# Optimization experiments

Hardware: AMD Instinct MI355X
Metric: run time of the kernel (lower is better)

Reference implementation:

```python
import jax, jax.numpy as jnp
import numpy as np

B, S, D = 4, 2048, 1024


def setup_inputs() -> dict:
    key = jax.random.key(0)
    ks = jax.random.split(key, 9)
    scale = 1.0 / np.sqrt(D)
    x = jax.random.normal(ks[0], (B, S, D), dtype=jnp.float32)
    # causal mask (batch, seq, seq), int32; positions with 0 are masked out
    mask = jnp.broadcast_to(jnp.tril(jnp.ones((S, S), dtype=jnp.int32)), (B, S, S))
    Wq = jax.random.uniform(ks[1], (D, D), jnp.float32, -scale, scale)
    bq = jax.random.uniform(ks[2], (D,), jnp.float32, -scale, scale)
    Wk = jax.random.uniform(ks[3], (D, D), jnp.float32, -scale, scale)
    bk = jax.random.uniform(ks[4], (D,), jnp.float32, -scale, scale)
    Wv = jax.random.uniform(ks[5], (D, D), jnp.float32, -scale, scale)
    bv = jax.random.uniform(ks[6], (D,), jnp.float32, -scale, scale)
    Wo = jax.random.uniform(ks[7], (D, D), jnp.float32, -scale, scale)
    bo = jax.random.uniform(ks[8], (D,), jnp.float32, -scale, scale)
    return {"x": x, "mask": mask, "Wq": Wq, "bq": bq, "Wk": Wk, "bk": bk,
            "Wv": Wv, "bv": bv, "Wo": Wo, "bo": bo}


def reference(x, mask, Wq, bq, Wk, bk, Wv, bv, Wo, bo):
    d_model = x.shape[-1]
    scaling = jnp.sqrt(jnp.asarray(d_model, dtype=jnp.float32))
    # torch nn.Linear: y = x @ W.T + b
    Q = jnp.einsum('bsd,ed->bse', x, Wq) + bq
    K = jnp.einsum('bsd,ed->bse', x, Wk) + bk
    V = jnp.einsum('bsd,ed->bse', x, Wv) + bv
    scores = jnp.einsum('bqd,bkd->bqk', Q, K) / scaling  # (B, S, S)
    scores = jnp.where(mask == 0, jnp.float32(-1e9), scores)
    attn = jax.nn.softmax(scores, axis=2)
    out = jnp.einsum('bqk,bkd->bqd', attn, V)
    out = jnp.einsum('bsd,ed->bse', out, Wo) + bo
    return out, attn
```

## Files before the change

kernel.cpp:

```cpp
#include <hip/hip_runtime.h>
#include <hip/hip_bf16.h>
#include <stdint.h>


typedef unsigned short u16;
typedef __attribute__((ext_vector_type(8))) __bf16 bf16x8;
typedef __attribute__((ext_vector_type(4))) float f32x4;

__device__ __forceinline__ u16 f2bf(float f) {
  unsigned int u = __builtin_bit_cast(unsigned int, f);
  u = u + 0x7FFFu + ((u >> 16) & 1u);
  return (u16)(u >> 16);
}

__device__ __forceinline__ float bf2f(u16 u) {
  unsigned int w = ((unsigned int)u) << 16;
  return __builtin_bit_cast(float, w);
}

__device__ __forceinline__ void gl_lds16(const void* g, void* l) {
  __builtin_amdgcn_global_load_lds(
      (const __attribute__((address_space(1))) void*)g,
      (__attribute__((address_space(3))) void*)l, 16, 0, 0);
}

#define MFMA(a, b, c) __builtin_amdgcn_mfma_f32_16x16x32_bf16((a), (b), (c), 0, 0, 0)

#define TILE 128
#define BKK  64
template<int GM, int GX, int OUTMODE, bool BIAS, bool CKB, int NTT>
__global__ __launch_bounds__(256) void gemm_bt(
    const u16* __restrict__ A, const u16* __restrict__ Bmat,
    const float* __restrict__ b0, const float* __restrict__ b1,
    const float* __restrict__ b2,
    void* __restrict__ C0, u16* __restrict__ C1, u16* __restrict__ C2,
    int N, int K, long long sAb, long long sBb, long long sCb, int nchunk,
    const u16* __restrict__ A6, const u16* __restrict__ B6,
    u16* __restrict__ C6) {
  __shared__ __align__(16) u16 As[2][TILE * BKK];
  __shared__ __align__(16) u16 Bs[2][TILE * BKK];
  const int bid = blockIdx.x;
  int bx, by, bz;
  int role6 = 0;
  if (GM == 1) {
    const int lidx = (bid & 7) * nchunk + (bid >> 3);
    bz = lidx / 136;
    const int i = lidx - bz * 136;
    by = (int)((sqrtf(8.f * i + 1.f) - 1.f) * 0.5f);
    while ((by + 1) * (by + 2) / 2 <= i) ++by;
    while (by * (by + 1) / 2 > i) --by;
    bx = i - by * (by + 1) / 2;
  } else if (GM == 3) {
    const int j = bid & 255;
    const int k = j >> 5;
    by = (bid >> 8) ? k : 15 - k;
    bz = (j & 31) >> 3;
    bx = j & 7;
  } else if (GM == 4) {
    const int xcd = bid & 7, c = bid >> 3;
    bz = 0;
    by = xcd * 8 + (c >> 3);
    bx = c & 7;
  } else {
    const int lidx = (bid & 7) * nchunk + (bid >> 3);
    if (lidx < 544) {
      bz = lidx / 136;
      const int i = lidx - bz * 136;
      by = (int)((sqrtf(8.f * i + 1.f) - 1.f) * 0.5f);
      while ((by + 1) * (by + 2) / 2 <= i) ++by;
      while (by * (by + 1) / 2 > i) --by;
      bx = i - by * (by + 1) / 2;
    } else {
      role6 = 1;
      const int v = lidx - 544;
      bz = v >> 7;
      by = (v & 127) >> 4;
      bx = v & 15;
    }
  }
  const int t = threadIdx.x;
  const int lane = t & 63, wid = t >> 6;
  const int wm = (wid >> 1) * 64, wn = (wid & 1) * 64;
  const int fr = lane & 15, fh = lane >> 4;

  const u16* Aeff = A;
  const u16* Beff = Bmat;
  u16* C0e = (u16*)C0;
  long long sAe = sAb, sBe = sBb, sCe = sCb;
  if (GM == 6 && role6) {
    Aeff = A6; Beff = B6; C0e = C6;
    sAe = 0;
    sCe = (long long)1024 * 2048;
  }

  const char* Ab = (const char*)(Aeff + (size_t)bz * sAe + (size_t)by * TILE * K);
  const size_t rowstride = (size_t)K * 2;
  const size_t BOFF = (size_t)8 * TILE * rowstride;
  const char* Btile = (const char*)(Beff + (size_t)bz * sBe + (size_t)bx * TILE * K);

  int srow[4], scol[4], slin[4];
#pragma unroll
  for (int c = 0; c < 4; ++c) {
    slin[c] = c * 4096 + t * 16;
    srow[c] = slin[c] >> 7;
    scol[c] = (slin[c] & 127) ^ ((srow[c] & 7) << 4);
  }

  int Keff = K;
  if (CKB) { int kb2 = (by + 1) * TILE; Keff = kb2 < K ? kb2 : K; }
  const int nkt = Keff / BKK;

#define STAGE(ko_, buf_, Bp_)                                                 \
  {                                                                           \
    _Pragma("unroll") for (int c = 0; c < 4; ++c) {                           \
      gl_lds16(Ab + (size_t)srow[c] * rowstride + (ko_) + scol[c],            \
               (char*)As[buf_] + slin[c]);                                    \
      gl_lds16((Bp_) + (size_t)srow[c] * rowstride + (ko_) + scol[c],         \
               (char*)Bs[buf_] + slin[c]);                                    \
    }                                                                         \
  }

  STAGE(0, 0, Btile)
  __syncthreads();

  int cur = 0;
  for (int tt = 0; tt < NTT; ++tt) {
    f32x4 acc[4][4];
#pragma unroll
    for (int m = 0; m < 4; ++m)
#pragma unroll
      for (int n = 0; n < 4; ++n) acc[m][n] = {0.f, 0.f, 0.f, 0.f};

    for (int kt = 0; kt < nkt; ++kt) {
      const bool last = (kt + 1 == nkt);
      if (!last) {
        STAGE((size_t)(kt + 1) * (BKK * 2), cur ^ 1, Btile)
      } else if (NTT > 1 && tt + 1 < NTT) {
        STAGE(0, cur ^ 1, Btile + BOFF)
      }
      const char* Ac = (const char*)As[cur];
      const char* Bc = (const char*)Bs[cur];
#pragma unroll
      for (int kk = 0; kk < BKK; kk += 32) {
        bf16x8 af[4], bg[4];
#pragma unroll
        for (int m = 0; m < 4; ++m) {
          int r = wm + m * 16 + fr;
          int cb = (kk * 2 + fh * 16) ^ ((r & 7) << 4);
          af[m] = *(const bf16x8*)(Ac + r * 128 + cb);
        }
#pragma unroll
        for (int n = 0; n < 4; ++n) {
          int r = wn + n * 16 + fr;
          int cb = (kk * 2 + fh * 16) ^ ((r & 7) << 4);
          bg[n] = *(const bf16x8*)(Bc + r * 128 + cb);
        }
#pragma unroll
        for (int m = 0; m < 4; ++m)
#pragma unroll
          for (int n = 0; n < 4; ++n)
            acc[m][n] = MFMA(af[m], bg[n], acc[m][n]);
      }
      if (!last) __syncthreads();
      cur ^= 1;
    }

    const int bxe = bx + 8 * tt;
    const int gm0 = by * TILE + wm, gn0 = bxe * TILE + wn;
#pragma unroll
    for (int n = 0; n < 4; ++n) {
      const int gc = gn0 + n * 16 + fr;
      float bvv = 0.f;
      if (BIAS) {
        if (OUTMODE == 3) {
          const int w = bxe >> 3;
          bvv = (w == 0 ? b0 : w == 1 ? b1 : b2)[gc & 1023];
        } else {
          bvv = b0[gc];
        }
      }
#pragma unroll
      for (int m = 0; m < 4; ++m) {
        const int gr0 = gm0 + m * 16 + fh * 4;
        float v[4];
#pragma unroll
        for (int j = 0; j < 4; ++j) v[j] = acc[m][n][j] + bvv;
        if (OUTMODE == 1) {
          float* C = (float*)C0 + (size_t)bz * sCb;
#pragma unroll
          for (int j = 0; j < 4; ++j) C[(size_t)(gr0 + j) * N + gc] = v[j];
        } else if (OUTMODE == 0) {
          u16* C = C0e + (size_t)bz * sCe;
#pragma unroll
          for (int j = 0; j < 4; ++j) C[(size_t)(gr0 + j) * N + gc] = f2bf(v[j]);
        } else {
          const int w = bxe >> 3;
          const int gcl = gc & 1023;
          u16* dst = (w == 0) ? (u16*)C0 : (w == 1) ? C1 : C2;
          const float sc = (w == 0) ? 0.03125f : 1.0f;
#pragma unroll
          for (int j = 0; j < 4; ++j)
            dst[(size_t)(gr0 + j) * 1024 + gcl] = f2bf(v[j] * sc);
        }
      }
    }

    if (NTT > 1 && tt + 1 < NTT) {
      __syncthreads();
      Btile += BOFF;
    }
  }
#undef STAGE
}

__global__ __launch_bounds__(256) void cvt_all(
    const float4* __restrict__ x, ushort4* __restrict__ xb,
    const float4* __restrict__ w0, const float4* __restrict__ w1,
    const float4* __restrict__ w2, const float4* __restrict__ w3,
    ushort4* __restrict__ o0, ushort4* __restrict__ o1,
    ushort4* __restrict__ o2, ushort4* __restrict__ o3) {
  int i = blockIdx.x * 256 + threadIdx.x;
  const float4* src;
  ushort4* dst;
  int idx;
  if (i < 2097152) {
    src = x; dst = xb; idx = i;
  } else {
    int j = i - 2097152;
    int w = j >> 18;
    idx = j & 262143;
    src = (w == 0) ? w0 : (w == 1) ? w1 : (w == 2) ? w2 : w3;
    dst = (w == 0) ? o0 : (w == 1) ? o1 : (w == 2) ? o2 : o3;
  }
  float4 v = src[idx];
  ushort4 o;
  o.x = f2bf(v.x); o.y = f2bf(v.y); o.z = f2bf(v.z); o.w = f2bf(v.w);
  dst[idx] = o;
}

__global__ __launch_bounds__(256) void softmax_rows(
    u16* __restrict__ pb, float* __restrict__ attnF) {
  const int row = blockIdx.x;
  const int q = row & 2047;
  const int nv = q + 1;
  const int nvt = (q & ~127) + 128;
  const int t = threadIdx.x;
  u16* brow = pb + (size_t)row * 2048;
  float* srow = attnF + (size_t)row * 2048;
  __shared__ float red[4];

  const int e0 = 8 * t;
  float a[8];
  if (e0 < nvt) {
    ushort4 u0 = ((const ushort4*)brow)[2 * t];
    ushort4 u1 = ((const ushort4*)brow)[2 * t + 1];
    u16 us[8] = {u0.x, u0.y, u0.z, u0.w, u1.x, u1.y, u1.z, u1.w};
#pragma unroll
    for (int j = 0; j < 8; ++j)
      a[j] = (e0 + j < nv) ? bf2f(us[j]) : -3.0e38f;
  } else {
#pragma unroll
    for (int j = 0; j < 8; ++j) a[j] = -3.0e38f;
  }

  float lmax = -3.0e38f;
#pragma unroll
  for (int j = 0; j < 8; ++j) lmax = fmaxf(lmax, a[j]);
#pragma unroll
  for (int o = 32; o > 0; o >>= 1) lmax = fmaxf(lmax, __shfl_xor(lmax, o));
  if ((t & 63) == 0) red[t >> 6] = lmax;
  __syncthreads();
  const float m = fmaxf(fmaxf(red[0], red[1]), fmaxf(red[2], red[3]));
  __syncthreads();

  float lsum = 0.f;
#pragma unroll
  for (int j = 0; j < 8; ++j) {
    a[j] = __expf(a[j] - m);
    lsum += a[j];
  }
#pragma unroll
  for (int o = 32; o > 0; o >>= 1) lsum += __shfl_xor(lsum, o);
  if ((t & 63) == 0) red[t >> 6] = lsum;
  __syncthreads();
  const float inv = 1.f / (red[0] + red[1] + red[2] + red[3]);

#pragma unroll
  for (int j = 0; j < 8; ++j) a[j] *= inv;
  ((float4*)srow)[2 * t]     = float4{a[0], a[1], a[2], a[3]};
  ((float4*)srow)[2 * t + 1] = float4{a[4], a[5], a[6], a[7]};
  if (e0 < nvt) {
    ushort4 ba; ba.x = f2bf(a[0]); ba.y = f2bf(a[1]); ba.z = f2bf(a[2]); ba.w = f2bf(a[3]);
    ushort4 bb; bb.x = f2bf(a[4]); bb.y = f2bf(a[5]); bb.z = f2bf(a[6]); bb.w = f2bf(a[7]);
    ((ushort4*)brow)[2 * t]     = ba;
    ((ushort4*)brow)[2 * t + 1] = bb;
  }
}

extern "C" void kernel_launch(void* const* d_in, const int* in_sizes, int n_in,
                              void* d_out, int out_size, void* d_ws,
                              size_t ws_size, hipStream_t stream) {
  (void)in_sizes; (void)n_in; (void)out_size; (void)ws_size;
  const int B = 4, S = 2048, D = 1024;
  const float* x  = (const float*)d_in[0];
  const float* Wq = (const float*)d_in[2]; const float* bq = (const float*)d_in[3];
  const float* Wk = (const float*)d_in[4]; const float* bk = (const float*)d_in[5];
  const float* Wv = (const float*)d_in[6]; const float* bv = (const float*)d_in[7];
  const float* Wo = (const float*)d_in[8]; const float* bo = (const float*)d_in[9];

  float* out  = (float*)d_out;
  float* attn = out + (size_t)B * S * D;

  char* ws = (char*)d_ws;
  u16* xb  = (u16*)(ws);
  u16* wqb = (u16*)(ws + 16777216);
  u16* wkb = wqb + 1048576;
  u16* wvb = wkb + 1048576;
  u16* wob = wvb + 1048576;
  u16* qb  = (u16*)(ws + 25165824);
  u16* kb  = (u16*)(ws + 41943040);
  u16* vr  = (u16*)(ws + 58720256);
  u16* pb  = (u16*)(ws + 75497472);

  cvt_all<<<12288, 256, 0, stream>>>(
      (const float4*)x, (ushort4*)xb,
      (const float4*)Wq, (const float4*)Wk, (const float4*)Wv, (const float4*)Wo,
      (ushort4*)wqb, (ushort4*)wkb, (ushort4*)wvb, (ushort4*)wob);

  gemm_bt<4, 24, 3, true, false, 3><<<512, 256, 0, stream>>>(
      xb, wqb, bq, bk, bv, qb, kb, vr, 3072, 1024, 0, 0, 0, 0,
      nullptr, nullptr, nullptr);

  gemm_bt<6, 1, 0, false, false, 1><<<1056, 256, 0, stream>>>(
      qb, kb, nullptr, nullptr, nullptr, pb, nullptr, nullptr,
      2048, 1024, (long long)S * D, (long long)S * D, (long long)S * S, 132,
      wob, vr, xb);

  softmax_rows<<<B * S, 256, 0, stream>>>(pb, attn);

  gemm_bt<3, 8, 1, true, true, 1><<<512, 256, 0, stream>>>(
      pb, xb, bo, nullptr, nullptr, out, nullptr, nullptr,
      1024, 2048, (long long)S * S, (long long)D * S, (long long)S * D, 0,
      nullptr, nullptr, nullptr);
}
```

Baseline: 187.7 us.

## Split-K the long causal rows of the final GEMM with atomic accumulation

The last GEMM (P·(VWo) producing the output) now gives each upper-half row tile (by>=8), whose causal K extent is long, two K-halves handled by separate blocks. Those blocks accumulate into the fp32 output with atomicAdd, and only the first half adds the bias. The conversion kernel gets extra blocks that zero the corresponding output region first. The aim is to even out load imbalance from the triangular K range and raise the block count from 512 to 768. The cost is atomic traffic, an extra zeroing pass, and fp32 summation order that is no longer deterministic.

```diff
diff --git a/kernel.cpp b/kernel.cpp
--- a/kernel.cpp
+++ b/kernel.cpp
@@ -42,6 +42,7 @@
   const int bid = blockIdx.x;
   int bx, by, bz;
   int role6 = 0;
+  int ks9 = 0;
   if (GM == 1) {
     const int lidx = (bid & 7) * nchunk + (bid >> 3);
     bz = lidx / 136;
@@ -50,17 +51,25 @@
     while ((by + 1) * (by + 2) / 2 <= i) ++by;
     while (by * (by + 1) / 2 > i) --by;
     bx = i - by * (by + 1) / 2;
-  } else if (GM == 3) {
-    const int j = bid & 255;
-    const int k = j >> 5;
-    by = (bid >> 8) ? k : 15 - k;
-    bz = (j & 31) >> 3;
-    bx = j & 7;
   } else if (GM == 4) {
     const int xcd = bid & 7, c = bid >> 3;
     bz = 0;
     by = xcd * 8 + (c >> 3);
     bx = c & 7;
+  } else if (GM == 9) {
+    const int i9 = bid / 96, r9 = bid - i9 * 96;
+    if (r9 < 64) {
+      by = 15 - i9;
+      ks9 = r9 & 1;
+      const int j2 = r9 >> 1;
+      bz = j2 >> 3;
+      bx = j2 & 7;
+    } else {
+      by = 7 - i9;
+      const int u = r9 - 64;
+      bz = u >> 3;
+      bx = u & 7;
+    }
   } else {
     const int lidx = (bid & 7) * nchunk + (bid >> 3);
     if (lidx < 544) {
@@ -106,9 +115,17 @@
     scol[c] = (slin[c] & 127) ^ ((srow[c] & 7) << 4);
   }
 
-  int Keff = K;
-  if (CKB) { int kb2 = (by + 1) * TILE; Keff = kb2 < K ? kb2 : K; }
-  const int nkt = Keff / BKK;
+  int nkt, kb0 = 0;
+  if (GM == 9) {
+    if (by >= 8) { nkt = by + 1; kb0 = ks9 * nkt; }
+    else nkt = (by + 1) * 2;
+  } else {
+    int Keff = K;
+    if (CKB) { int kb2 = (by + 1) * TILE; Keff = kb2 < K ? kb2 : K; }
+    nkt = Keff / BKK;
+  }
+  Ab += (size_t)kb0 * (BKK * 2);
+  Btile += (size_t)kb0 * (BKK * 2);
 
 #define STAGE(ko_, buf_, Bp_)                                                 \
   {                                                                           \
@@ -179,6 +196,7 @@
           bvv = b0[gc];
         }
       }
+      if (GM == 9 && by >= 8 && ks9 != 0) bvv = 0.f;
 #pragma unroll
       for (int m = 0; m < 4; ++m) {
         const int gr0 = gm0 + m * 16 + fh * 4;
@@ -187,8 +205,14 @@
         for (int j = 0; j < 4; ++j) v[j] = acc[m][n][j] + bvv;
         if (OUTMODE == 1) {
           float* C = (float*)C0 + (size_t)bz * sCb;
-#pragma unroll
-          for (int j = 0; j < 4; ++j) C[(size_t)(gr0 + j) * N + gc] = v[j];
+          if (GM == 9 && by >= 8) {
+#pragma unroll
+            for (int j = 0; j < 4; ++j)
+              atomicAdd(&C[(size_t)(gr0 + j) * N + gc], v[j]);
+          } else {
+#pragma unroll
+            for (int j = 0; j < 4; ++j) C[(size_t)(gr0 + j) * N + gc] = v[j];
+          }
         } else if (OUTMODE == 0) {
           u16* C = C0e + (size_t)bz * sCe;
 #pragma unroll
@@ -218,7 +242,16 @@
     const float4* __restrict__ w0, const float4* __restrict__ w1,
     const float4* __restrict__ w2, const float4* __restrict__ w3,
     ushort4* __restrict__ o0, ushort4* __restrict__ o1,
-    ushort4* __restrict__ o2, ushort4* __restrict__ o3) {
+    ushort4* __restrict__ o2, ushort4* __restrict__ o3,
+    float* __restrict__ oz) {
+  if (blockIdx.x >= 12288) {
+    const int u = (blockIdx.x - 12288) * 256 + threadIdx.x;
+    const int bz2 = u >> 16, r = u & 65535;
+    float4 z = {0.f, 0.f, 0.f, 0.f};
+    float4* dst = (float4*)oz + (size_t)bz2 * 524288 + 262144 + (size_t)r * 4;
+    dst[0] = z; dst[1] = z; dst[2] = z; dst[3] = z;
+    return;
+  }
   int i = blockIdx.x * 256 + threadIdx.x;
   const float4* src;
   ushort4* dst;
@@ -322,10 +355,10 @@
   u16* vr  = (u16*)(ws + 58720256);
   u16* pb  = (u16*)(ws + 75497472);
 
-  cvt_all<<<12288, 256, 0, stream>>>(
+  cvt_all<<<13312, 256, 0, stream>>>(
       (const float4*)x, (ushort4*)xb,
       (const float4*)Wq, (const float4*)Wk, (const float4*)Wv, (const float4*)Wo,
-      (ushort4*)wqb, (ushort4*)wkb, (ushort4*)wvb, (ushort4*)wob);
+      (ushort4*)wqb, (ushort4*)wkb, (ushort4*)wvb, (ushort4*)wob, out);
 
   gemm_bt<4, 24, 3, true, false, 3><<<512, 256, 0, stream>>>(
       xb, wqb, bq, bk, bv, qb, kb, vr, 3072, 1024, 0, 0, 0, 0,
@@ -338,7 +371,7 @@
 
   softmax_rows<<<B * S, 256, 0, stream>>>(pb, attn);
 
-  gemm_bt<3, 8, 1, true, true, 1><<<512, 256, 0, stream>>>(
+  gemm_bt<9, 8, 1, true, false, 1><<<768, 256, 0, stream>>>(
       pb, xb, bo, nullptr, nullptr, out, nullptr, nullptr,
       1024, 2048, (long long)S * S, (long long)D * S, (long long)S * D, 0,
       nullptr, nullptr, nullptr);
```

New measurement: 205.1 us. +9.3%, slower.
